# Performance work log

Hardware: AMD Instinct MI355X
Metric: run time of the kernel (lower is better)

The kernel has to match this reference:

```python
import jax, jax.numpy as jnp
import numpy as np

NUM_CODES = 8192
DIM = 256
DECAY = 0.99
EPS = 1e-05


def setup_inputs() -> dict:
    key = jax.random.key(0)
    k1, k2, k3, k4 = jax.random.split(key, 4)
    z = jax.random.normal(k1, (8, 16, 128, DIM), dtype=jnp.float32)
    codebook = jax.random.normal(k2, (NUM_CODES, DIM), dtype=jnp.float32)
    ema_count = jax.random.uniform(k3, (NUM_CODES,), dtype=jnp.float32)
    ema_mean = jax.random.normal(k4, (NUM_CODES, DIM), dtype=jnp.float32)
    return {"z": z, "codebook": codebook, "ema_count": ema_count, "ema_mean": ema_mean}


def reference(z, codebook, ema_count, ema_mean):
    B, C, P, D = z.shape
    flat = z.reshape(-1, D)  # [N, D]
    dist = (jnp.sum(flat * flat, axis=1, keepdims=True)
            - 2.0 * flat @ codebook.T
            + jnp.sum(codebook * codebook, axis=1)[None, :])  # [N, K]
    idx = jnp.argmin(dist, axis=1)  # [N]
    z_q = codebook[idx].reshape(B, C, P, D)

    # --- training-mode EMA update (segment_sum instead of one-hot matmul) ---
    counts = jax.ops.segment_sum(jnp.ones_like(idx, dtype=flat.dtype), idx,
                                 num_segments=NUM_CODES)  # onehot.sum(0)
    mean = jax.ops.segment_sum(flat, idx, num_segments=NUM_CODES)  # onehot.T @ flat
    new_count = DECAY * ema_count + (1.0 - DECAY) * counts
    new_mean = DECAY * ema_mean + (1.0 - DECAY) * mean
    n = jnp.sum(new_count)
    cluster_size = (new_count + EPS) / (n + NUM_CODES * EPS) * n
    new_codebook = new_mean / cluster_size[:, None]

    # losses use z_q from the pre-update codebook (as in the torch forward)
    loss = jnp.mean((jax.lax.stop_gradient(z_q) - z) ** 2) \
         + 0.25 * jnp.mean((z_q - jax.lax.stop_gradient(z)) ** 2)
    z_q_st = jax.lax.stop_gradient(z_q) + (z - jax.lax.stop_gradient(z))
    return (z_q_st, loss, idx.reshape(B, C, P), new_codebook, new_count, new_mean)
```

## Files before the change

kernel.cpp:

```cpp
#include <hip/hip_runtime.h>

#define N_ROWS 16384
#define DIM    256
#define K_CODES 8192

#define QSCALE (127.0f / 5.5f)

#define OFF_ZQ   0
#define OFF_LOSS 4194304
#define OFF_IDX  4194305
#define OFF_CB   4210689
#define OFF_CNT  6307841
#define OFF_MEAN 6316033

#define POFF_ZQP   0
#define POFF_CQP   1048576
#define POFF_CAND  4210692
#define POFF_BROWS 4210692
#define POFF_BCODE 4227076

#define WS_CNT    0
#define WS_CN8    32768
#define WS_LOSSP  65536
#define WS_N      81920
#define WS_MEAN   98304
#define WS_CUR    8486912
#define WS_ROWC   8519680

typedef int i32x4 __attribute__((ext_vector_type(4)));
typedef float f32x4 __attribute__((ext_vector_type(4)));

__device__ inline signed char q8(float v) {
    float x = v * QSCALE;
    x = fminf(fmaxf(x, -127.0f), 127.0f);
    return (signed char)__float2int_rn(x);
}

__global__ __launch_bounds__(256) void prep_kernel(const float* __restrict__ z,
                                                   const float* __restrict__ cb,
                                                   signed char* __restrict__ zqp,
                                                   signed char* __restrict__ cqp,
                                                   unsigned* __restrict__ cn8,
                                                   float* __restrict__ meanAcc,
                                                   unsigned* __restrict__ counts) {
    int b = blockIdx.x;
    if (b < 1024) {
        int g = b * 256 + threadIdx.x;
        int row = g >> 4, gr = g & 15;
        const float* src = z + (size_t)row * DIM + gr * 16;
        char cq[16];
        #pragma unroll
        for (int t = 0; t < 4; ++t) {
            float4 v = *(const float4*)(src + t * 4);
            cq[t * 4 + 0] = q8(v.x); cq[t * 4 + 1] = q8(v.y);
            cq[t * 4 + 2] = q8(v.z); cq[t * 4 + 3] = q8(v.w);
        }
        int zblk = row >> 7, r = row & 127, kc = gr >> 2, gk = gr & 3;
        size_t o = ((size_t)((zblk * 4 + kc) * 4 + gk) * 128 + r) * 16;
        *(i32x4*)(zqp + o) = *(const i32x4*)cq;
    } else if (b < 3072) {
        int w = threadIdx.x >> 6, lane = threadIdx.x & 63;
        int row = (b - 1024) * 4 + w;
        float4 v = *(const float4*)(cb + (size_t)row * DIM + lane * 4);
        char cq[4] = {q8(v.x), q8(v.y), q8(v.z), q8(v.w)};
        int gr = lane >> 2;
        int kc = gr >> 2, gk = gr & 3;
        int cblk = row >> 8, r = row & 255;
        size_t o = ((size_t)((cblk * 4 + kc) * 4 + gk) * 256 + r) * 16 + (lane & 3) * 4;
        *(int*)(cqp + o) = *(const int*)cq;
        int s = (int)cq[0] * cq[0] + (int)cq[1] * cq[1] + (int)cq[2] * cq[2] + (int)cq[3] * cq[3];
        #pragma unroll
        for (int off = 32; off; off >>= 1) s += __shfl_down(s, off, 64);
        if (lane == 0) cn8[row] = ((unsigned)(s + 16777216)) << 7;
    } else if (b < 4096) {
        int g = (b - 3072) * 256 + threadIdx.x;
        float4 zero = {0.f, 0.f, 0.f, 0.f};
        float4* p = (float4*)(meanAcc + (size_t)g * 8);
        p[0] = zero; p[1] = zero;
    } else {
        #pragma unroll
        for (int i = 0; i < 32; ++i) counts[threadIdx.x * 32 + i] = 0u;
    }
}

__global__ __launch_bounds__(256, 3) void dist_kernel(const signed char* __restrict__ zqp,
                                                      const signed char* __restrict__ cqp,
                                                      const unsigned* __restrict__ cn8,
                                                      unsigned* __restrict__ cand) {
    __shared__ unsigned red[4][64][2];

    const int tid = threadIdx.x;
    const int w = tid >> 6, lane = tid & 63;
    const int c16 = lane & 15, g4 = lane >> 4;

    int b = blockIdx.x;
    int xcd = b & 7;
    int wgx = b >> 3;
    int cbY = wgx >> 5;
    int zbX = xcd * 32 + (wgx & 31);

    i32x4 acc[4][4];
    #pragma unroll
    for (int i = 0; i < 4; ++i)
        #pragma unroll
        for (int j = 0; j < 4; ++j) acc[i][j] = 0;

    const signed char* Abase = cqp + (size_t)cbY * 65536 + g4 * 4096 + (w * 64 + c16) * 16;
    const signed char* Bbase = zqp + (size_t)(zbX >> 1) * 32768 + g4 * 2048 + ((zbX & 1) * 64 + c16) * 16;

    i32x4 a[4], b_[4], an[4], bn[4];
    #pragma unroll
    for (int i = 0; i < 4; ++i) a[i] = *(const i32x4*)(Abase + i * 256);
    #pragma unroll
    for (int j = 0; j < 4; ++j) b_[j] = *(const i32x4*)(Bbase + j * 256);

    #pragma unroll
    for (int kc = 0; kc < 4; ++kc) {
        if (kc < 3) {
            #pragma unroll
            for (int i = 0; i < 4; ++i) an[i] = *(const i32x4*)(Abase + (kc + 1) * 16384 + i * 256);
            #pragma unroll
            for (int j = 0; j < 4; ++j) bn[j] = *(const i32x4*)(Bbase + (kc + 1) * 8192 + j * 256);
            __builtin_amdgcn_sched_barrier(0);
        }
        #pragma unroll
        for (int i = 0; i < 4; ++i)
            #pragma unroll
            for (int j = 0; j < 4; ++j)
                acc[i][j] = __builtin_amdgcn_mfma_i32_16x16x64_i8(a[i], b_[j], acc[i][j], 0, 0, 0);
        if (kc < 3) {
            __builtin_amdgcn_sched_barrier(0);
            #pragma unroll
            for (int i = 0; i < 4; ++i) a[i] = an[i];
            #pragma unroll
            for (int j = 0; j < 4; ++j) b_[j] = bn[j];
        }
    }

    unsigned cn[4][4];
    #pragma unroll
    for (int i = 0; i < 4; ++i)
        #pragma unroll
        for (int reg = 0; reg < 4; ++reg)
            cn[i][reg] = cn8[cbY * 256 + w * 64 + i * 16 + g4 * 4 + reg];

    #pragma unroll
    for (int j = 0; j < 4; ++j) {
        unsigned b1 = 0xFFFFFFFFu, b2 = 0xFFFFFFFFu;
        #pragma unroll
        for (int i = 0; i < 4; ++i) {
            #pragma unroll
            for (int reg = 0; reg < 4; ++reg) {
                unsigned id = (unsigned)(w * 64 + i * 16 + g4 * 4 + reg);
                unsigned key = ((cn[i][reg] - ((unsigned)acc[i][j][reg] << 8)) & 0xFFFFFF00u) | id;
                unsigned mx = max(b1, key);
                b1 = min(b1, key);
                b2 = min(b2, mx);
            }
        }
        #pragma unroll
        for (int off = 16; off <= 32; off <<= 1) {
            unsigned o1 = __shfl_xor(b1, off), o2 = __shfl_xor(b2, off);
            unsigned m1 = min(b1, o1);
            unsigned hi = max(b1, o1);
            b1 = m1;
            b2 = min(min(b2, o2), hi);
        }
        if (lane < 16) { red[w][j * 16 + lane][0] = b1; red[w][j * 16 + lane][1] = b2; }
    }
    __syncthreads();
    if (tid < 64) {
        unsigned b1 = 0xFFFFFFFFu, b2 = 0xFFFFFFFFu;
        #pragma unroll
        for (int t = 0; t < 4; ++t) {
            unsigned o1 = red[t][tid][0], o2 = red[t][tid][1];
            unsigned m1 = min(b1, o1);
            unsigned hi = max(b1, o1);
            b1 = m1;
            b2 = min(min(b2, o2), hi);
        }
        size_t base = (size_t)(zbX * 64 + tid) * 64 + cbY * 2;
        *(uint2*)(cand + base) = make_uint2(b1, b2);
    }
}

__global__ __launch_bounds__(256) void rescore_kernel(const float* __restrict__ z,
                                                      const float* __restrict__ cb,
                                                      const unsigned* __restrict__ cand,
                                                      float* __restrict__ zq_out,
                                                      float* __restrict__ idx_out,
                                                      unsigned* __restrict__ rowcode,
                                                      unsigned* __restrict__ counts,
                                                      float* __restrict__ lossPart) {
    __shared__ float lred[4];
    int w = threadIdx.x >> 6, lane = threadIdx.x & 63;
    int row = blockIdx.x * 4 + w;
    unsigned k32 = cand[(size_t)row * 64 + lane];
    unsigned m = k32;
    #pragma unroll
    for (int off = 32; off; off >>= 1) {
        unsigned o = __shfl_xor(m, off);
        if (o < m) m = o;
    }
    unsigned vmin = m >> 8;
    unsigned vme = k32 >> 8;
    int mycode = (lane >> 1) * 256 + (int)(k32 & 0xFFu);
    unsigned long long mask = __ballot(vme <= vmin + 1400u);

    float4 zv = *(const float4*)(z + (size_t)row * DIM + lane * 4);
    double bd = 1e300;
    int bc = 0x7fffffff;
    while (mask) {
        int src = __ffsll((unsigned long long)mask) - 1;
        mask &= mask - 1;
        int code = __shfl(mycode, src);
        float4 c4 = *(const float4*)(cb + (size_t)code * DIM + lane * 4);
        double d0 = (double)zv.x - c4.x, d1 = (double)zv.y - c4.y;
        double d2 = (double)zv.z - c4.z, d3 = (double)zv.w - c4.w;
        double s = d0 * d0 + d1 * d1 + d2 * d2 + d3 * d3;
        #pragma unroll
        for (int off = 32; off; off >>= 1) s += __shfl_xor(s, off);
        if (s < bd || (s == bd && code < bc)) { bd = s; bc = code; }
    }

    float4 cv = *(const float4*)(cb + (size_t)bc * DIM + lane * 4);
    *(float4*)(zq_out + (size_t)row * DIM + lane * 4) = cv;
    if (lane == 0) {
        idx_out[row] = (float)bc;
        rowcode[row] = (unsigned)bc;
        atomicAdd(counts + bc, 1u);
        lred[w] = (float)bd;
    }
    __syncthreads();
    if (threadIdx.x == 0)
        lossPart[blockIdx.x] = lred[0] + lred[1] + lred[2] + lred[3];
}

__global__ __launch_bounds__(1024) void prefix_kernel(const unsigned* __restrict__ counts,
                                                      const float* __restrict__ ema_count,
                                                      const float* __restrict__ lossPart,
                                                      unsigned* __restrict__ cursor,
                                                      float* __restrict__ newCount_out,
                                                      float* __restrict__ nOut,
                                                      float* __restrict__ loss_out) {
    __shared__ unsigned ssum[1024];
    __shared__ float fred[1024];
    const float OMD = 0.01f;
    int tid = threadIdx.x;
    int base = tid * 8;

    unsigned v[8];
    unsigned s = 0;
    float es = 0.f;
    #pragma unroll
    for (int i = 0; i < 8; ++i) {
        v[i] = counts[base + i];
        s += v[i];
        float e = ema_count[base + i];
        es += e;
        newCount_out[base + i] = 0.99f * e + OMD * (float)v[i];
    }
    ssum[tid] = s;
    __syncthreads();
    for (int off = 1; off < 1024; off <<= 1) {
        unsigned t = (tid >= off) ? ssum[tid - off] : 0u;
        __syncthreads();
        ssum[tid] += t;
        __syncthreads();
    }
    unsigned run = ssum[tid] - s;
    #pragma unroll
    for (int i = 0; i < 8; ++i) {
        cursor[base + i] = run;
        run += v[i];
    }

    fred[tid] = es;
    __syncthreads();
    for (int off = 512; off; off >>= 1) {
        if (tid < off) fred[tid] += fred[tid + off];
        __syncthreads();
    }
    if (tid == 0) nOut[0] = 0.99f * fred[0] + OMD * (float)N_ROWS;
    __syncthreads();
    float L = lossPart[tid] + lossPart[tid + 1024] + lossPart[tid + 2048] + lossPart[tid + 3072];
    fred[tid] = L;
    __syncthreads();
    for (int off = 512; off; off >>= 1) {
        if (tid < off) fred[tid] += fred[tid + off];
        __syncthreads();
    }
    if (tid == 0) loss_out[0] = 1.25f * fred[0] / 4194304.0f;
}

__global__ __launch_bounds__(256) void scatter_kernel(const unsigned* __restrict__ rowcode,
                                                      unsigned* __restrict__ cursor,
                                                      unsigned* __restrict__ bucketRows,
                                                      unsigned* __restrict__ bucketCodes) {
    int row = blockIdx.x * 256 + threadIdx.x;
    unsigned code = rowcode[row];
    unsigned pos = atomicAdd(cursor + code, 1u);
    bucketRows[pos] = row;
    bucketCodes[pos] = code;
}

__global__ __launch_bounds__(256) void bucket_sum_kernel(const float* __restrict__ z,
                                                         const unsigned* __restrict__ bucketRows,
                                                         const unsigned* __restrict__ bucketCodes,
                                                         float* __restrict__ meanAcc) {
    int w = threadIdx.x >> 6, lane = threadIdx.x & 63;
    int base = (blockIdx.x * 4 + w) * 8;

    float4 acc = {0.f, 0.f, 0.f, 0.f};
    unsigned cur = bucketCodes[base];
    #pragma unroll
    for (int e = 0; e < 8; ++e) {
        int p = base + e;
        unsigned code = bucketCodes[p];
        if (code != cur) {
            float* mp = meanAcc + (size_t)cur * DIM + lane * 4;
            atomicAdd(mp + 0, acc.x);
            atomicAdd(mp + 1, acc.y);
            atomicAdd(mp + 2, acc.z);
            atomicAdd(mp + 3, acc.w);
            acc.x = acc.y = acc.z = acc.w = 0.f;
            cur = code;
        }
        unsigned r = bucketRows[p];
        float4 zv = *(const float4*)(z + (size_t)r * DIM + lane * 4);
        acc.x += zv.x; acc.y += zv.y; acc.z += zv.z; acc.w += zv.w;
    }
    float* mp = meanAcc + (size_t)cur * DIM + lane * 4;
    atomicAdd(mp + 0, acc.x);
    atomicAdd(mp + 1, acc.y);
    atomicAdd(mp + 2, acc.z);
    atomicAdd(mp + 3, acc.w);
}

__global__ __launch_bounds__(256) void merge_kernel(const float* __restrict__ ema_mean,
                                                    const float* __restrict__ meanAcc,
                                                    const float* __restrict__ newCount,
                                                    const float* __restrict__ nPtr,
                                                    float* __restrict__ newMean_out,
                                                    float* __restrict__ newCb_out) {
    int g = blockIdx.x * 256 + threadIdx.x;
    int k = g >> 6;
    int c4 = (g & 63) * 4;
    float n = nPtr[0];
    float nc = newCount[k];
    float cs = (nc + 1e-5f) / (n + (float)(K_CODES * 1e-5)) * n;
    size_t base = (size_t)k * DIM + c4;
    float4 em = *(const float4*)(ema_mean + base);
    float4 mm = *(const float4*)(meanAcc + base);
    float4 nm;
    nm.x = 0.99f * em.x + 0.01f * mm.x;
    nm.y = 0.99f * em.y + 0.01f * mm.y;
    nm.z = 0.99f * em.z + 0.01f * mm.z;
    nm.w = 0.99f * em.w + 0.01f * mm.w;
    *(float4*)(newMean_out + base) = nm;
    float4 cbv;
    cbv.x = nm.x / cs;
    cbv.y = nm.y / cs;
    cbv.z = nm.z / cs;
    cbv.w = nm.w / cs;
    *(float4*)(newCb_out + base) = cbv;
}

extern "C" void kernel_launch(void* const* d_in, const int* in_sizes, int n_in,
                              void* d_out, int out_size, void* d_ws, size_t ws_size,
                              hipStream_t stream) {
    const float* z         = (const float*)d_in[0];
    const float* cb        = (const float*)d_in[1];
    const float* ema_count = (const float*)d_in[2];
    const float* ema_mean  = (const float*)d_in[3];
    float* out = (float*)d_out;
    char* ws = (char*)d_ws;

    unsigned* counts  = (unsigned*)(ws + WS_CNT);
    unsigned* cn8     = (unsigned*)(ws + WS_CN8);
    float* lossPart   = (float*)(ws + WS_LOSSP);
    float* nPtr       = (float*)(ws + WS_N);
    float* meanAcc    = (float*)(ws + WS_MEAN);
    unsigned* cursor  = (unsigned*)(ws + WS_CUR);
    unsigned* rowcode = (unsigned*)(ws + WS_ROWC);

    signed char* zqp = (signed char*)(out + POFF_ZQP);
    signed char* cqp = (signed char*)(out + POFF_CQP);
    unsigned* cand  = (unsigned*)(out + POFF_CAND);
    unsigned* brows = (unsigned*)(out + POFF_BROWS);
    unsigned* bcode = (unsigned*)(out + POFF_BCODE);

    prep_kernel<<<4097, 256, 0, stream>>>(z, cb, zqp, cqp, cn8, meanAcc, counts);
    dist_kernel<<<8192, 256, 0, stream>>>(zqp, cqp, cn8, cand);
    rescore_kernel<<<N_ROWS / 4, 256, 0, stream>>>(z, cb, cand, out + OFF_ZQ, out + OFF_IDX,
                                                   rowcode, counts, lossPart);
    prefix_kernel<<<1, 1024, 0, stream>>>(counts, ema_count, lossPart, cursor,
                                          out + OFF_CNT, nPtr, out + OFF_LOSS);
    scatter_kernel<<<N_ROWS / 256, 256, 0, stream>>>(rowcode, cursor, brows, bcode);
    bucket_sum_kernel<<<512, 256, 0, stream>>>(z, brows, bcode, meanAcc);
    merge_kernel<<<(K_CODES * DIM / 4) / 256, 256, 0, stream>>>(ema_mean, meanAcc,
                                                                out + OFF_CNT, nPtr,
                                                                out + OFF_MEAN, out + OFF_CB);
}
```

Measured before the change: 116.9 us.

## Fuse segment-sum into rescore via direct per-row atomic adds, drop bucket sort

Each rescore wave now atomically adds its row's z vector into the assigned code's mean accumulator. This removes the prefix-scan, scatter and bucket-sum kernels, and the prefix kernel shrinks to a count/loss finalizer. It saves two launches plus the rowcode/bucket traffic. In exchange every row issues 256 float atomics instead of pre-aggregated ones, which adds atomic traffic and contention on popular codes, and the order of float accumulation is no longer deterministic.

Measured after the change: 159.0 us. 1.36x slower.

```diff
diff --git a/kernel.cpp b/kernel.cpp
--- a/kernel.cpp
+++ b/kernel.cpp
@@ -16,16 +16,12 @@
 #define POFF_ZQP   0
 #define POFF_CQP   1048576
 #define POFF_CAND  4210692
-#define POFF_BROWS 4210692
-#define POFF_BCODE 4227076
 
 #define WS_CNT    0
 #define WS_CN8    32768
 #define WS_LOSSP  65536
 #define WS_N      81920
 #define WS_MEAN   98304
-#define WS_CUR    8486912
-#define WS_ROWC   8519680
 
 typedef int i32x4 __attribute__((ext_vector_type(4)));
 typedef float f32x4 __attribute__((ext_vector_type(4)));
@@ -184,14 +180,14 @@
     }
 }
 
-__global__ __launch_bounds__(256) void rescore_kernel(const float* __restrict__ z,
-                                                      const float* __restrict__ cb,
-                                                      const unsigned* __restrict__ cand,
-                                                      float* __restrict__ zq_out,
-                                                      float* __restrict__ idx_out,
-                                                      unsigned* __restrict__ rowcode,
-                                                      unsigned* __restrict__ counts,
-                                                      float* __restrict__ lossPart) {
+__global__ __launch_bounds__(256) void rescore_assign_kernel(const float* __restrict__ z,
+                                                             const float* __restrict__ cb,
+                                                             const unsigned* __restrict__ cand,
+                                                             float* __restrict__ zq_out,
+                                                             float* __restrict__ idx_out,
+                                                             unsigned* __restrict__ counts,
+                                                             float* __restrict__ meanAcc,
+                                                             float* __restrict__ lossPart) {
     __shared__ float lred[4];
     int w = threadIdx.x >> 6, lane = threadIdx.x & 63;
     int row = blockIdx.x * 4 + w;
@@ -225,9 +221,13 @@
 
     float4 cv = *(const float4*)(cb + (size_t)bc * DIM + lane * 4);
     *(float4*)(zq_out + (size_t)row * DIM + lane * 4) = cv;
+    float* mp = meanAcc + (size_t)bc * DIM + lane * 4;
+    atomicAdd(mp + 0, zv.x);
+    atomicAdd(mp + 1, zv.y);
+    atomicAdd(mp + 2, zv.z);
+    atomicAdd(mp + 3, zv.w);
     if (lane == 0) {
         idx_out[row] = (float)bc;
-        rowcode[row] = (unsigned)bc;
         atomicAdd(counts + bc, 1u);
         lred[w] = (float)bd;
     }
@@ -236,45 +236,24 @@
         lossPart[blockIdx.x] = lred[0] + lred[1] + lred[2] + lred[3];
 }
 
-__global__ __launch_bounds__(1024) void prefix_kernel(const unsigned* __restrict__ counts,
-                                                      const float* __restrict__ ema_count,
-                                                      const float* __restrict__ lossPart,
-                                                      unsigned* __restrict__ cursor,
-                                                      float* __restrict__ newCount_out,
-                                                      float* __restrict__ nOut,
-                                                      float* __restrict__ loss_out) {
-    __shared__ unsigned ssum[1024];
+__global__ __launch_bounds__(1024) void count_final_kernel(const unsigned* __restrict__ counts,
+                                                           const float* __restrict__ ema_count,
+                                                           const float* __restrict__ lossPart,
+                                                           float* __restrict__ newCount_out,
+                                                           float* __restrict__ nOut,
+                                                           float* __restrict__ loss_out) {
     __shared__ float fred[1024];
     const float OMD = 0.01f;
     int tid = threadIdx.x;
     int base = tid * 8;
 
-    unsigned v[8];
-    unsigned s = 0;
     float es = 0.f;
     #pragma unroll
     for (int i = 0; i < 8; ++i) {
-        v[i] = counts[base + i];
-        s += v[i];
         float e = ema_count[base + i];
         es += e;
-        newCount_out[base + i] = 0.99f * e + OMD * (float)v[i];
-    }
-    ssum[tid] = s;
-    __syncthreads();
-    for (int off = 1; off < 1024; off <<= 1) {
-        unsigned t = (tid >= off) ? ssum[tid - off] : 0u;
-        __syncthreads();
-        ssum[tid] += t;
-        __syncthreads();
-    }
-    unsigned run = ssum[tid] - s;
-    #pragma unroll
-    for (int i = 0; i < 8; ++i) {
-        cursor[base + i] = run;
-        run += v[i];
-    }
-
+        newCount_out[base + i] = 0.99f * e + OMD * (float)counts[base + i];
+    }
     fred[tid] = es;
     __syncthreads();
     for (int off = 512; off; off >>= 1) {
@@ -291,50 +270,6 @@
         __syncthreads();
     }
     if (tid == 0) loss_out[0] = 1.25f * fred[0] / 4194304.0f;
-}
-
-__global__ __launch_bounds__(256) void scatter_kernel(const unsigned* __restrict__ rowcode,
-                                                      unsigned* __restrict__ cursor,
-                                                      unsigned* __restrict__ bucketRows,
-                                                      unsigned* __restrict__ bucketCodes) {
-    int row = blockIdx.x * 256 + threadIdx.x;
-    unsigned code = rowcode[row];
-    unsigned pos = atomicAdd(cursor + code, 1u);
-    bucketRows[pos] = row;
-    bucketCodes[pos] = code;
-}
-
-__global__ __launch_bounds__(256) void bucket_sum_kernel(const float* __restrict__ z,
-                                                         const unsigned* __restrict__ bucketRows,
-                                                         const unsigned* __restrict__ bucketCodes,
-                                                         float* __restrict__ meanAcc) {
-    int w = threadIdx.x >> 6, lane = threadIdx.x & 63;
-    int base = (blockIdx.x * 4 + w) * 8;
-
-    float4 acc = {0.f, 0.f, 0.f, 0.f};
-    unsigned cur = bucketCodes[base];
-    #pragma unroll
-    for (int e = 0; e < 8; ++e) {
-        int p = base + e;
-        unsigned code = bucketCodes[p];
-        if (code != cur) {
-            float* mp = meanAcc + (size_t)cur * DIM + lane * 4;
-            atomicAdd(mp + 0, acc.x);
-            atomicAdd(mp + 1, acc.y);
-            atomicAdd(mp + 2, acc.z);
-            atomicAdd(mp + 3, acc.w);
-            acc.x = acc.y = acc.z = acc.w = 0.f;
-            cur = code;
-        }
-        unsigned r = bucketRows[p];
-        float4 zv = *(const float4*)(z + (size_t)r * DIM + lane * 4);
-        acc.x += zv.x; acc.y += zv.y; acc.z += zv.z; acc.w += zv.w;
-    }
-    float* mp = meanAcc + (size_t)cur * DIM + lane * 4;
-    atomicAdd(mp + 0, acc.x);
-    atomicAdd(mp + 1, acc.y);
-    atomicAdd(mp + 2, acc.z);
-    atomicAdd(mp + 3, acc.w);
 }
 
 __global__ __launch_bounds__(256) void merge_kernel(const float* __restrict__ ema_mean,
@@ -381,23 +316,18 @@
     float* lossPart   = (float*)(ws + WS_LOSSP);
     float* nPtr       = (float*)(ws + WS_N);
     float* meanAcc    = (float*)(ws + WS_MEAN);
-    unsigned* cursor  = (unsigned*)(ws + WS_CUR);
-    unsigned* rowcode = (unsigned*)(ws + WS_ROWC);
 
     signed char* zqp = (signed char*)(out + POFF_ZQP);
     signed char* cqp = (signed char*)(out + POFF_CQP);
     unsigned* cand  = (unsigned*)(out + POFF_CAND);
-    unsigned* brows = (unsigned*)(out + POFF_BROWS);
-    unsigned* bcode = (unsigned*)(out + POFF_BCODE);
 
     prep_kernel<<<4097, 256, 0, stream>>>(z, cb, zqp, cqp, cn8, meanAcc, counts);
     dist_kernel<<<8192, 256, 0, stream>>>(zqp, cqp, cn8, cand);
-    rescore_kernel<<<N_ROWS / 4, 256, 0, stream>>>(z, cb, cand, out + OFF_ZQ, out + OFF_IDX,
-                                                   rowcode, counts, lossPart);
-    prefix_kernel<<<1, 1024, 0, stream>>>(counts, ema_count, lossPart, cursor,
-                                          out + OFF_CNT, nPtr, out + OFF_LOSS);
-    scatter_kernel<<<N_ROWS / 256, 256, 0, stream>>>(rowcode, cursor, brows, bcode);
-    bucket_sum_kernel<<<512, 256, 0, stream>>>(z, brows, bcode, meanAcc);
+    rescore_assign_kernel<<<N_ROWS / 4, 256, 0, stream>>>(z, cb, cand, out + OFF_ZQ,
+                                                          out + OFF_IDX, counts, meanAcc,
+                                                          lossPart);
+    count_final_kernel<<<1, 1024, 0, stream>>>(counts, ema_count, lossPart,
+                                               out + OFF_CNT, nPtr, out + OFF_LOSS);
     merge_kernel<<<(K_CODES * DIM / 4) / 256, 256, 0, stream>>>(ema_mean, meanAcc,
                                                                 out + OFF_CNT, nPtr,
                                                                 out + OFF_MEAN, out + OFF_CB);
```
